# Kernel optimization log

Measured on AMD Instinct MI355X. Metric: run time of the kernel, lower is better.

The kernel has to match this reference:

```python
import jax, jax.numpy as jnp
import numpy as np
import math

# --- config (OctoConfig defaults) ---
OBS_H = 2
STATE_DIM = 2
N_LAYER = 12
N_HEAD = 6
N_EMBD = 384
IMG = 96
PATCH = 8
N_IMG_TOK = (IMG // PATCH) ** 2          # 144
TOT_TOK = OBS_H * (N_IMG_TOK + 1) + 1    # 291
HEAD_DIM = N_EMBD // N_HEAD
LN_EPS = 1e-5
B = 128


def _sinusoidal_pos_embed(n_position, d_hid):
    position = np.arange(n_position)[:, None].astype(np.float32)
    div_term = np.exp(np.arange(0, d_hid, 2).astype(np.float32) * -(math.log(10000.0) / d_hid))
    pe = np.zeros((1, n_position, d_hid), dtype=np.float32)
    pe[0, :, 0::2] = np.sin(position * div_term)
    pe[0, :, 1::2] = np.cos(position * div_term)
    return jnp.asarray(pe)


def setup_inputs() -> dict:
    key = jax.random.key(0)
    ks = jax.random.split(key, 16)
    std = 0.02
    inp = {}
    inp['images'] = jax.random.normal(ks[0], (B, OBS_H, 3, IMG, IMG), jnp.float32)
    inp['agent_state'] = jax.random.normal(ks[1], (B, OBS_H, STATE_DIM), jnp.float32)
    # image tokenizer
    inp['img_proj_w'] = jax.random.normal(ks[2], (PATCH * PATCH * 3, N_EMBD), jnp.float32) * std
    inp['img_proj_b'] = jnp.zeros((N_EMBD,), jnp.float32)
    inp['img_temb'] = jax.random.normal(ks[3], (1, OBS_H, 1, N_EMBD), jnp.float32)
    # agent-state tokenizer MLP: state_dim -> 32 -> n_embd
    inp['st_w1'] = jax.random.normal(ks[4], (STATE_DIM, 32), jnp.float32) * std
    inp['st_b1'] = jnp.zeros((32,), jnp.float32)
    inp['st_w2'] = jax.random.normal(ks[5], (32, N_EMBD), jnp.float32) * std
    inp['st_b2'] = jnp.zeros((N_EMBD,), jnp.float32)
    inp['st_temb'] = jax.random.normal(ks[6], (1, OBS_H, 1, N_EMBD), jnp.float32)
    inp['readout'] = jax.random.normal(ks[7], (1, 1, N_EMBD), jnp.float32)
    inp['pos_embed'] = _sinusoidal_pos_embed(TOT_TOK, N_EMBD)
    # stacked per-layer transformer params (leading dim = N_LAYER), scanned
    L = N_LAYER
    inp['ln1_w'] = jnp.ones((L, N_EMBD), jnp.float32)
    inp['ln1_b'] = jnp.zeros((L, N_EMBD), jnp.float32)
    inp['attn_w'] = jax.random.normal(ks[8], (L, N_EMBD, 3 * N_EMBD), jnp.float32) * std
    inp['attn_b'] = jnp.zeros((L, 3 * N_EMBD), jnp.float32)
    inp['attn_proj_w'] = jax.random.normal(ks[9], (L, N_EMBD, N_EMBD), jnp.float32) * std
    inp['attn_proj_b'] = jnp.zeros((L, N_EMBD), jnp.float32)
    inp['ln2_w'] = jnp.ones((L, N_EMBD), jnp.float32)
    inp['ln2_b'] = jnp.zeros((L, N_EMBD), jnp.float32)
    inp['fc_w'] = jax.random.normal(ks[10], (L, N_EMBD, 4 * N_EMBD), jnp.float32) * std
    inp['fc_b'] = jnp.zeros((L, 4 * N_EMBD), jnp.float32)
    inp['fc2_w'] = jax.random.normal(ks[11], (L, 4 * N_EMBD, N_EMBD), jnp.float32) * std
    inp['fc2_b'] = jnp.zeros((L, N_EMBD), jnp.float32)
    inp['lnf_w'] = jnp.ones((N_EMBD,), jnp.float32)
    inp['lnf_b'] = jnp.zeros((N_EMBD,), jnp.float32)
    return inp


def _layernorm(x, w, b):
    m = jnp.mean(x, axis=-1, keepdims=True)
    v = jnp.mean((x - m) ** 2, axis=-1, keepdims=True)
    return (x - m) * jax.lax.rsqrt(v + LN_EPS) * w + b


def _forward(images, agent_state, img_proj_w, img_proj_b, img_temb,
             st_w1, st_b1, st_w2, st_b2, st_temb, readout, pos_embed,
             ln1_w, ln1_b, attn_w, attn_b, attn_proj_w, attn_proj_b,
             ln2_w, ln2_b, fc_w, fc_b, fc2_w, fc2_b, lnf_w, lnf_b):
    Bn, T, C, H, W = images.shape
    p = PATCH
    # --- ImageTokenizer: patchify (B*T, n_patches, p*p*C) then project ---
    x = images.reshape(Bn * T, C, H // p, p, W // p, p)
    x = x.transpose(0, 2, 4, 3, 5, 1).reshape(Bn * T, -1, p * p * C)
    img_tok = x @ img_proj_w + img_proj_b
    img_tok = img_tok.reshape(Bn, T, -1, N_EMBD) + img_temb  # [B,T,144,D]
    # --- AgentStateTokenizer ---
    st = jax.nn.relu(agent_state @ st_w1 + st_b1) @ st_w2 + st_b2
    st_tok = st.reshape(Bn, T, 1, N_EMBD) + st_temb          # [B,T,1,D]
    # --- combine + readout + positional ---
    combined = jnp.concatenate([st_tok, img_tok], axis=2).reshape(Bn, -1, N_EMBD)
    ro = jnp.broadcast_to(readout, (Bn, 1, N_EMBD))
    x = jnp.concatenate([combined, ro], axis=1) + pos_embed  # [B,291,D]
    Ttot = x.shape[1]
    # custom mask: all-visible except last (readout) row attends only to itself
    neg = jnp.float32(-jnp.inf)
    bias = jnp.zeros((Ttot, Ttot), jnp.float32).at[-1, :-1].set(neg)
    scale = 1.0 / math.sqrt(HEAD_DIM + 1e-8)

    def block(h, params):
        (l1w, l1b, aw, ab, pw, pb, l2w, l2b, fw, fb, f2w, f2b) = params
        y = _layernorm(h, l1w, l1b)
        qkv = y @ aw + ab
        q, k, v = jnp.split(qkv, 3, axis=-1)
        q = q.reshape(Bn, Ttot, N_HEAD, HEAD_DIM)
        k = k.reshape(Bn, Ttot, N_HEAD, HEAD_DIM)
        v = v.reshape(Bn, Ttot, N_HEAD, HEAD_DIM)
        scores = jnp.einsum('bqhd,bkhd->bhqk', q, k) * scale + bias
        attn = jax.nn.softmax(scores, axis=-1)
        o = jnp.einsum('bhqk,bkhd->bqhd', attn, v).reshape(Bn, Ttot, N_EMBD)
        h = h + o @ pw + pb
        y2 = _layernorm(h, l2w, l2b)
        h = h + jax.nn.gelu(y2 @ fw + fb, approximate=True) @ f2w + f2b
        return h, None

    layer_params = (ln1_w, ln1_b, attn_w, attn_b, attn_proj_w, attn_proj_b,
                    ln2_w, ln2_b, fc_w, fc_b, fc2_w, fc2_b)
    x, _ = jax.lax.scan(block, x, layer_params)
    x = _layernorm(x, lnf_w, lnf_b)
    return x[:, -1]  # readout token embedding [B, D]


def reference(images, agent_state, img_proj_w, img_proj_b, img_temb,
              st_w1, st_b1, st_w2, st_b2, st_temb, readout, pos_embed,
              ln1_w, ln1_b, attn_w, attn_b, attn_proj_w, attn_proj_b,
              ln2_w, ln2_b, fc_w, fc_b, fc2_w, fc2_b, lnf_w, lnf_b):
    return _forward(images, agent_state, img_proj_w, img_proj_b, img_temb,
                    st_w1, st_b1, st_w2, st_b2, st_temb, readout, pos_embed,
                    ln1_w, ln1_b, attn_w, attn_b, attn_proj_w, attn_proj_b,
                    ln2_w, ln2_b, fc_w, fc_b, fc2_w, fc2_b, lnf_w, lnf_b)
```

## Files before the change

kernel.cpp:

```cpp
#include <hip/hip_runtime.h>

typedef unsigned short u16;
typedef unsigned int u32;

typedef __bf16 bf16x8 __attribute__((ext_vector_type(8)));
typedef float  f32x4  __attribute__((ext_vector_type(4)));

#define N_EMBD 384
#define TT     291
#define NB     128

__device__ __forceinline__ u16 f2bf(float x) {
    union { float f; u32 u; } v; v.f = x;
    u32 r = v.u + 0x7FFFu + ((v.u >> 16) & 1u);
    return (u16)(r >> 16);
}
__device__ __forceinline__ float bfl(u32 u) { return __uint_as_float(u << 16); }
__device__ __forceinline__ float bfh(u32 u) { return __uint_as_float(u & 0xFFFF0000u); }

__device__ __forceinline__ float gelu_f(float x) {
    float u = 0.7978845608028654f * x * (1.f + 0.044715f * x * x);
    float e = __expf(2.f * u);
    float t = 1.f - 2.f / (e + 1.f);
    return 0.5f * x * (1.f + t);
}

__device__ __forceinline__ void load16_lds(const u16* g, u16* l) {
    __builtin_amdgcn_global_load_lds(
        (const __attribute__((address_space(1))) u32*)g,
        (__attribute__((address_space(3))) u32*)l, 16, 0, 0);
}

__device__ __forceinline__ void tr_tile(const float* __restrict__ src,
                                        u16* __restrict__ dst,
                                        int R, int C, int r0, int c0, int tid) {
    __shared__ float tile[32][33];
    int cc = tid & 31, rr0 = tid >> 5;
#pragma unroll
    for (int s = 0; s < 4; ++s) {
        int rr = rr0 + s * 8;
        tile[rr][cc] = src[(size_t)(r0 + rr) * C + c0 + cc];
    }
    __syncthreads();
#pragma unroll
    for (int s = 0; s < 4; ++s) {
        int rr = rr0 + s * 8;
        dst[(size_t)(c0 + rr) * R + (r0 + cc)] = f2bf(tile[cc][rr]);
    }
}

__global__ __launch_bounds__(256) void transpose_cvt(const float* __restrict__ in,
                                                     u16* __restrict__ out, int R, int C) {
    tr_tile(in, out, R, C, blockIdx.y * 32, blockIdx.x * 32, threadIdx.x);
}

__global__ __launch_bounds__(256) void transpose_layer(const float* __restrict__ attn_w,
                                                       const float* __restrict__ proj_w,
                                                       const float* __restrict__ fc_w,
                                                       const float* __restrict__ fc2_w,
                                                       u16* __restrict__ wqkv,
                                                       u16* __restrict__ wproj,
                                                       u16* __restrict__ wfc,
                                                       u16* __restrict__ wfc2t,
                                                       int l) {
    int t = blockIdx.x;
    const float* src; u16* dst; int R, C, tx, ty;
    if (t < 432)       { int i = t;        src = attn_w + (size_t)l * 384 * 1152; dst = wqkv;  R = 384;  C = 1152; tx = i % 36; ty = i / 36; }
    else if (t < 576)  { int i = t - 432;  src = proj_w + (size_t)l * 384 * 384;  dst = wproj; R = 384;  C = 384;  tx = i % 12; ty = i / 12; }
    else if (t < 1152) { int i = t - 576;  src = fc_w   + (size_t)l * 384 * 1536; dst = wfc;   R = 384;  C = 1536; tx = i % 48; ty = i / 48; }
    else               { int i = t - 1152; src = fc2_w  + (size_t)l * 1536 * 384; dst = wfc2t; R = 1536; C = 384;  tx = i % 12; ty = i / 12; }
    tr_tile(src, dst, R, C, ty * 32, tx * 32, threadIdx.x);
}

template<int MODE>
__global__ __launch_bounds__(256) void gemm_bt(const u16* __restrict__ A,
                                               const u16* __restrict__ BT, int ldb,
                                               const float* __restrict__ bias,
                                               void* __restrict__ out,
                                               const float* __restrict__ resid,
                                               int N, int K) {
    __shared__ u16 As[128 * 64];
    __shared__ u16 Bs[128 * 64];
    int tid = threadIdx.x;
    int lane = tid & 63, wave = tid >> 6;
    int wr = wave >> 1, wc = wave & 1;

    int nwg  = gridDim.x * gridDim.y;
    int orig = blockIdx.y * gridDim.x + blockIdx.x;
    int qq = nwg >> 3, rr = nwg & 7;
    int xcd = orig & 7, idx0 = orig >> 3;
    int wg = (xcd < rr ? xcd * (qq + 1) : rr * (qq + 1) + (xcd - rr) * qq) + idx0;
    int bx = wg % gridDim.x, by = wg / gridDim.x;

    const u16* Ab = A  + (size_t)by * 128 * K;
    const u16* Bb = BT + (size_t)bx * 128 * ldb;

    f32x4 acc[4][4];
#pragma unroll
    for (int i = 0; i < 4; ++i)
#pragma unroll
        for (int j = 0; j < 4; ++j)
#pragma unroll
            for (int r = 0; r < 4; ++r) acc[i][j][r] = 0.f;

    int r16  = lane & 15;
    int quad = lane >> 4;
    int sw   = r16 & 7;

    int srow[4], scol[4];
#pragma unroll
    for (int s = 0; s < 4; ++s) {
        int seg = s * 256 + tid;
        srow[s] = seg >> 3;
        scol[s] = (((seg & 7) ^ (srow[s] & 7)) << 3);
    }

    for (int kt = 0; kt < K; kt += 64) {
#pragma unroll
        for (int s = 0; s < 4; ++s) {
            int seg = s * 256 + tid;
            load16_lds(Ab + (size_t)srow[s] * K   + kt + scol[s], &As[seg * 8]);
            load16_lds(Bb + (size_t)srow[s] * ldb + kt + scol[s], &Bs[seg * 8]);
        }
        __syncthreads();
#pragma unroll
        for (int kk = 0; kk < 2; ++kk) {
            bf16x8 af[4], bff[4];
#pragma unroll
            for (int i = 0; i < 4; ++i) {
                int cg = ((kk * 4 + quad) ^ sw) << 3;
                af[i]  = *(const bf16x8*)&As[(wr * 64 + i * 16 + r16) * 64 + cg];
                bff[i] = *(const bf16x8*)&Bs[(wc * 64 + i * 16 + r16) * 64 + cg];
            }
#pragma unroll
            for (int i = 0; i < 4; ++i)
#pragma unroll
                for (int j = 0; j < 4; ++j)
                    acc[i][j] = __builtin_amdgcn_mfma_f32_16x16x32_bf16(af[i], bff[j], acc[i][j], 0, 0, 0);
        }
        __syncthreads();
    }

    int rbase = (lane >> 4) * 4;
#pragma unroll
    for (int i = 0; i < 4; ++i) {
#pragma unroll
        for (int j = 0; j < 4; ++j) {
            int gr0 = by * 128 + wr * 64 + i * 16 + rbase;
            int gc  = bx * 128 + wc * 64 + j * 16 + (lane & 15);
            float bj = bias ? bias[gc] : 0.f;
#pragma unroll
            for (int r = 0; r < 4; ++r) {
                size_t idx = (size_t)(gr0 + r) * N + gc;
                float v = acc[i][j][r] + bj;
                if (MODE == 0)      ((u16*)out)[idx] = f2bf(v);
                else if (MODE == 1) ((u16*)out)[idx] = f2bf(gelu_f(v));
                else if (MODE == 2) ((float*)out)[idx] = resid[idx] + v;
                else                ((float*)out)[idx] = v;
            }
        }
    }
}

template<bool BF16OUT>
__global__ __launch_bounds__(256) void ln_kernel(const float* __restrict__ x,
                                                 const float* __restrict__ w,
                                                 const float* __restrict__ b,
                                                 void* __restrict__ yout,
                                                 int inRowMul, int inRowAdd, int nRows) {
    int row = blockIdx.x * 4 + (threadIdx.x >> 6);
    if (row >= nRows) return;
    const float* xr = x + ((size_t)row * inRowMul + inRowAdd) * N_EMBD;
    int lane = threadIdx.x & 63;
    float v[6], s = 0.f, s2 = 0.f;
#pragma unroll
    for (int i = 0; i < 6; ++i) {
        v[i] = xr[lane + 64 * i];
        s += v[i]; s2 += v[i] * v[i];
    }
#pragma unroll
    for (int off = 32; off > 0; off >>= 1) {
        s  += __shfl_down(s, off);
        s2 += __shfl_down(s2, off);
    }
    float mean = __shfl(s, 0) * (1.f / 384.f);
    float var  = __shfl(s2, 0) * (1.f / 384.f) - mean * mean;
    float rs = rsqrtf(var + 1e-5f);
#pragma unroll
    for (int i = 0; i < 6; ++i) {
        int c = lane + 64 * i;
        float o = (v[i] - mean) * rs * w[c] + b[c];
        if (BF16OUT) ((u16*)yout)[(size_t)row * N_EMBD + c] = f2bf(o);
        else         ((float*)yout)[(size_t)row * N_EMBD + c] = o;
    }
}

__global__ __launch_bounds__(512) void attn_mfma(const u16* __restrict__ qkv,
                                                 u16* __restrict__ o) {
    __shared__ __align__(16) u16 Ks[304 * 64];
    __shared__ __align__(16) u16 Vt[64 * 328];
    __shared__ __align__(16) u16 Ps[8 * 16 * 40];
    int h = blockIdx.x, b = blockIdx.y;
    int tid = threadIdx.x;
    int lane = tid & 63, wave = tid >> 6;
    int ln = lane & 15, quad = lane >> 4;
    int sw = ln & 7;
    const u16* base = qkv + (size_t)b * TT * 1152;

    for (int c = tid; c < 304 * 8; c += 512) {
        int row = c >> 3;
        int g   = (c & 7) ^ (row & 7);
        int srow = row < TT ? row : TT - 1;
        load16_lds(base + (size_t)srow * 1152 + 384 + h * 64 + g * 8, &Ks[c * 8]);
    }
    for (int s = tid; s < TT * 8; s += 512) {
        int dg = s / TT, k = s - dg * TT;
        uint4 v = *(const uint4*)(base + (size_t)k * 1152 + 768 + h * 64 + dg * 8);
        const u16* pv = (const u16*)&v;
#pragma unroll
        for (int j = 0; j < 8; ++j) Vt[(dg * 8 + j) * 328 + k] = pv[j];
    }
    for (int s = tid; s < 64 * 37; s += 512) {
        int d = s / 37, c2 = s - d * 37;
        Vt[d * 328 + TT + c2] = 0;
    }
    __syncthreads();

    for (int qt = wave; qt < 19; qt += 8) {
        int q0 = qt * 16;
        int qrow = q0 + ln; if (qrow > TT - 1) qrow = TT - 1;
        const u16* qp = base + (size_t)qrow * 1152 + h * 64;
        bf16x8 qf0 = *(const bf16x8*)(qp + quad * 8);
        bf16x8 qf1 = *(const bf16x8*)(qp + 32 + quad * 8);

        f32x4 sc[19];
#pragma unroll
        for (int kt = 0; kt < 19; ++kt) {
            const u16* kr = &Ks[(kt * 16 + ln) * 64];
            bf16x8 kb0 = *(const bf16x8*)&kr[(quad ^ sw) << 3];
            bf16x8 kb1 = *(const bf16x8*)&kr[((4 | quad) ^ sw) << 3];
            f32x4 z = {0.f, 0.f, 0.f, 0.f};
            z = __builtin_amdgcn_mfma_f32_16x16x32_bf16(qf0, kb0, z, 0, 0, 0);
            sc[kt] = __builtin_amdgcn_mfma_f32_16x16x32_bf16(qf1, kb1, z, 0, 0, 0);
        }

        const float C = 0.18033688011112042f;
        float linv[4];
#pragma unroll
        for (int r = 0; r < 4; ++r) {
            float m = -1e30f;
            if (qt == 18) {
                int q = q0 + quad * 4 + r;
#pragma unroll
                for (int kt = 0; kt < 19; ++kt) {
                    int key = kt * 16 + ln;
                    bool ok = (key < TT) && (q != TT - 1 || key == TT - 1);
                    float s = ok ? sc[kt][r] : -1e30f;
                    sc[kt][r] = s;
                    m = fmaxf(m, s);
                }
            } else {
#pragma unroll
                for (int kt = 0; kt < 18; ++kt) m = fmaxf(m, sc[kt][r]);
                float s = (288 + ln < TT) ? sc[18][r] : -1e30f;
                sc[18][r] = s;
                m = fmaxf(m, s);
            }
            m = fmaxf(m, __shfl_xor(m, 1));
            m = fmaxf(m, __shfl_xor(m, 2));
            m = fmaxf(m, __shfl_xor(m, 4));
            m = fmaxf(m, __shfl_xor(m, 8));
            float mc = m * C;
            float l = 0.f;
#pragma unroll
            for (int kt = 0; kt < 19; ++kt) {
                float p = __builtin_amdgcn_exp2f(fmaf(sc[kt][r], C, -mc));
                sc[kt][r] = p;
                l += p;
            }
            l += __shfl_xor(l, 1);
            l += __shfl_xor(l, 2);
            l += __shfl_xor(l, 4);
            l += __shfl_xor(l, 8);
            linv[r] = 1.f / l;
        }

        u16* Pw = &Ps[wave * 16 * 40];
        f32x4 of[4];
#pragma unroll
        for (int nt = 0; nt < 4; ++nt)
#pragma unroll
            for (int r = 0; r < 4; ++r) of[nt][r] = 0.f;
#pragma unroll
        for (int kt2 = 0; kt2 < 10; ++kt2) {
#pragma unroll
            for (int half = 0; half < 2; ++half) {
                int kt = kt2 * 2 + half;
#pragma unroll
                for (int r = 0; r < 4; ++r) {
                    float v = (kt < 19) ? sc[kt][r] : 0.f;
                    Pw[(quad * 4 + r) * 40 + half * 16 + ln] = f2bf(v);
                }
            }
            bf16x8 pa = *(const bf16x8*)&Pw[ln * 40 + quad * 8];
#pragma unroll
            for (int nt = 0; nt < 4; ++nt) {
                bf16x8 vb = *(const bf16x8*)&Vt[(nt * 16 + ln) * 328 + kt2 * 32 + quad * 8];
                of[nt] = __builtin_amdgcn_mfma_f32_16x16x32_bf16(pa, vb, of[nt], 0, 0, 0);
            }
        }

#pragma unroll
        for (int nt = 0; nt < 4; ++nt) {
#pragma unroll
            for (int r = 0; r < 4; ++r) {
                int q = q0 + quad * 4 + r;
                if (q < TT)
                    o[((size_t)(b * TT + q)) * N_EMBD + h * 64 + nt * 16 + ln] =
                        f2bf(of[nt][r] * linv[r]);
            }
        }
    }
}

__global__ __launch_bounds__(256) void patchify_kernel(const float* __restrict__ images,
                                                       u16* __restrict__ P) {
    int idx = blockIdx.x * 256 + threadIdx.x;
    int col = idx % 192, row = idx / 192;
    int p = row % 144, bt = row / 144;
    int c = col % 3, pp = col / 3;
    int pw = pp & 7, ph = pp >> 3;
    int hp = p / 12, wp = p % 12;
    float v = images[(((size_t)bt * 3 + c) * 96 + hp * 8 + ph) * 96 + wp * 8 + pw];
    P[idx] = f2bf(v);
}

__global__ __launch_bounds__(256) void img_scatter_kernel(const float* __restrict__ imgtok,
                                                          const float* __restrict__ temb,
                                                          const float* __restrict__ pos,
                                                          float* __restrict__ xw) {
    int idx = blockIdx.x * 256 + threadIdx.x;
    int n = idx % 384, row = idx / 384;
    int p = row % 144, bt = row / 144;
    int t = bt & 1, b = bt >> 1;
    int tok = t * 145 + 1 + p;
    xw[((size_t)b * TT + tok) * N_EMBD + n] =
        imgtok[idx] + temb[t * N_EMBD + n] + pos[(size_t)tok * N_EMBD + n];
}

__global__ __launch_bounds__(384) void st_kernel(const float* __restrict__ state,
                                                 const float* __restrict__ w1,
                                                 const float* __restrict__ b1,
                                                 const float* __restrict__ w2,
                                                 const float* __restrict__ b2,
                                                 const float* __restrict__ temb,
                                                 const float* __restrict__ pos,
                                                 float* __restrict__ xw) {
    int bt = blockIdx.x;
    int t = bt & 1, b = bt >> 1;
    int n = threadIdx.x;
    float s0 = state[bt * 2], s1 = state[bt * 2 + 1];
    float acc = b2[n];
#pragma unroll
    for (int j = 0; j < 32; ++j) {
        float hh = fmaxf(s0 * w1[j] + s1 * w1[32 + j] + b1[j], 0.f);
        acc += hh * w2[j * N_EMBD + n];
    }
    int tok = t * 145;
    xw[((size_t)b * TT + tok) * N_EMBD + n] =
        acc + temb[t * N_EMBD + n] + pos[(size_t)tok * N_EMBD + n];
}

__global__ __launch_bounds__(256) void ro_kernel(const float* __restrict__ readout,
                                                 const float* __restrict__ pos,
                                                 float* __restrict__ xw) {
    int idx = blockIdx.x * 256 + threadIdx.x;
    int n = idx % 384, b = idx / 384;
    xw[((size_t)b * TT + 290) * N_EMBD + n] = readout[n] + pos[(size_t)290 * N_EMBD + n];
}

extern "C" void kernel_launch(void* const* d_in, const int* in_sizes, int n_in,
                              void* d_out, int out_size, void* d_ws, size_t ws_size,
                              hipStream_t stream) {
    const float* images   = (const float*)d_in[0];
    const float* state    = (const float*)d_in[1];
    const float* img_w    = (const float*)d_in[2];
    const float* img_b    = (const float*)d_in[3];
    const float* img_temb = (const float*)d_in[4];
    const float* st_w1    = (const float*)d_in[5];
    const float* st_b1    = (const float*)d_in[6];
    const float* st_w2    = (const float*)d_in[7];
    const float* st_b2    = (const float*)d_in[8];
    const float* st_temb  = (const float*)d_in[9];
    const float* readout  = (const float*)d_in[10];
    const float* pos      = (const float*)d_in[11];
    const float* ln1_w    = (const float*)d_in[12];
    const float* ln1_b    = (const float*)d_in[13];
    const float* attn_w   = (const float*)d_in[14];
    const float* attn_b   = (const float*)d_in[15];
    const float* proj_w   = (const float*)d_in[16];
    const float* proj_b   = (const float*)d_in[17];
    const float* ln2_w    = (const float*)d_in[18];
    const float* ln2_b    = (const float*)d_in[19];
    const float* fc_w     = (const float*)d_in[20];
    const float* fc_b     = (const float*)d_in[21];
    const float* fc2_w    = (const float*)d_in[22];
    const float* fc2_b    = (const float*)d_in[23];
    const float* lnf_w    = (const float*)d_in[24];
    const float* lnf_b    = (const float*)d_in[25];

    char* ws = (char*)d_ws;
    float* XW   = (float*)(ws);
    u16*   Y    = (u16*)(ws + 57212928ull);
    u16*   SH   = (u16*)(ws + 85819392ull);
    u16*   QKV  = SH;
    u16*   G    = SH;
    u16*   P    = SH;
    float* IMGT = (float*)(ws + 85819392ull + 14155776ull);
    u16*   WQKVl  = (u16*)(ws + 171638784ull);
    u16*   WPROJl = (u16*)(ws + 172523520ull);
    u16*   WFCl   = (u16*)(ws + 172818432ull);
    u16*   WFC2Tl = (u16*)(ws + 173998080ull);
    u16*   WIMG   = (u16*)(ws + 175177728ull);

    transpose_cvt<<<dim3(12, 6), 256, 0, stream>>>(img_w, WIMG, 192, 384);
    patchify_kernel<<<27648, 256, 0, stream>>>(images, P);
    gemm_bt<3><<<dim3(3, 288), 256, 0, stream>>>(P, WIMG, 192, img_b, IMGT, nullptr, 384, 192);
    img_scatter_kernel<<<55296, 256, 0, stream>>>(IMGT, img_temb, pos, XW);
    st_kernel<<<256, 384, 0, stream>>>(state, st_w1, st_b1, st_w2, st_b2, st_temb, pos, XW);
    ro_kernel<<<192, 256, 0, stream>>>(readout, pos, XW);

    const size_t M0 = 18688;
    for (int l = 0; l < 12; ++l) {
        transpose_layer<<<1728, 256, 0, stream>>>(attn_w, proj_w, fc_w, fc2_w,
                                                  WQKVl, WPROJl, WFCl, WFC2Tl, l);
        ln_kernel<true><<<9312, 256, 0, stream>>>(XW, ln1_w + l * 384, ln1_b + l * 384, Y, 1, 0, 37248);
        gemm_bt<0><<<dim3(9, 291), 256, 0, stream>>>(Y, WQKVl, 384, attn_b + l * 1152,
                                                     QKV, nullptr, 1152, 384);
        attn_mfma<<<dim3(6, 128), 512, 0, stream>>>(QKV, Y);
        gemm_bt<2><<<dim3(3, 291), 256, 0, stream>>>(Y, WPROJl, 384, proj_b + l * 384,
                                                     XW, XW, 384, 384);
        ln_kernel<true><<<9312, 256, 0, stream>>>(XW, ln2_w + l * 384, ln2_b + l * 384, Y, 1, 0, 37248);
        gemm_bt<1><<<dim3(12, 146), 256, 0, stream>>>(Y, WFCl, 384, fc_b + l * 1536,
                                                      G, nullptr, 1536, 384);
        gemm_bt<2><<<dim3(3, 146), 256, 0, stream>>>(G, WFC2Tl, 1536, fc2_b + l * 384,
                                                     XW, XW, 384, 1536);
        gemm_bt<1><<<dim3(12, 145), 256, 0, stream>>>(Y + M0 * 384, WFCl, 384, fc_b + l * 1536,
                                                      G, nullptr, 1536, 384);
        gemm_bt<2><<<dim3(3, 145), 256, 0, stream>>>(G, WFC2Tl, 1536, fc2_b + l * 384,
                                                     XW + M0 * 384, XW + M0 * 384, 384, 1536);
    }
    ln_kernel<false><<<32, 256, 0, stream>>>(XW, lnf_w, lnf_b, d_out, TT, 290, 128);
}
```

Baseline: 4.385 ms.

## Compute transposed attention scores to feed P directly from registers

The QK^T MFMA now swaps operands so each lane holds scores for one query across 4 consecutive keys. The probabilities can then be converted to bf16 in registers and used directly as the A operand of 16x16x16 MFMAs for PV, removing the per-wave LDS staging buffer for P. Row max and sum reductions drop from 4 rows × 4 shuffles to 2 shuffles per lane, and the 1/l factor is redistributed with shuffles. It also sets a min-blocks launch bound, and it uses twice as many narrower MFMAs for PV and keeps 19 packed P vectors in registers, which adds register pressure.

```diff
diff --git a/kernel.cpp b/kernel.cpp
--- a/kernel.cpp
+++ b/kernel.cpp
@@ -5,6 +5,7 @@
 
 typedef __bf16 bf16x8 __attribute__((ext_vector_type(8)));
 typedef float  f32x4  __attribute__((ext_vector_type(4)));
+typedef short  s16x4  __attribute__((ext_vector_type(4)));
 
 #define N_EMBD 384
 #define TT     291
@@ -23,6 +24,20 @@
     float e = __expf(2.f * u);
     float t = 1.f - 2.f / (e + 1.f);
     return 0.5f * x * (1.f + t);
+}
+
+__device__ __forceinline__ f32x4 mfma16(s16x4 a, s16x4 b, f32x4 c) {
+#if __has_builtin(__builtin_amdgcn_mfma_f32_16x16x16bf16_1k)
+    return __builtin_amdgcn_mfma_f32_16x16x16bf16_1k(a, b, c, 0, 0, 0);
+#elif __has_builtin(__builtin_amdgcn_mfma_f32_16x16x16_bf16)
+    typedef __bf16 bf16x4v __attribute__((ext_vector_type(4)));
+    return __builtin_amdgcn_mfma_f32_16x16x16_bf16(__builtin_bit_cast(bf16x4v, a),
+                                                   __builtin_bit_cast(bf16x4v, b), c, 0, 0, 0);
+#else
+    f32x4 d = c;
+    asm("v_mfma_f32_16x16x16_bf16 %0, %1, %2, %0" : "+v"(d) : "v"(a), "v"(b));
+    return d;
+#endif
 }
 
 __device__ __forceinline__ void load16_lds(const u16* g, u16* l) {
@@ -195,11 +210,10 @@
     }
 }
 
-__global__ __launch_bounds__(512) void attn_mfma(const u16* __restrict__ qkv,
-                                                 u16* __restrict__ o) {
+__global__ __launch_bounds__(512, 4) void attn_mfma(const u16* __restrict__ qkv,
+                                                    u16* __restrict__ o) {
     __shared__ __align__(16) u16 Ks[304 * 64];
     __shared__ __align__(16) u16 Vt[64 * 328];
-    __shared__ __align__(16) u16 Ps[8 * 16 * 40];
     int h = blockIdx.x, b = blockIdx.y;
     int tid = threadIdx.x;
     int lane = tid & 63, wave = tid >> 6;
@@ -240,86 +254,81 @@
             bf16x8 kb0 = *(const bf16x8*)&kr[(quad ^ sw) << 3];
             bf16x8 kb1 = *(const bf16x8*)&kr[((4 | quad) ^ sw) << 3];
             f32x4 z = {0.f, 0.f, 0.f, 0.f};
-            z = __builtin_amdgcn_mfma_f32_16x16x32_bf16(qf0, kb0, z, 0, 0, 0);
-            sc[kt] = __builtin_amdgcn_mfma_f32_16x16x32_bf16(qf1, kb1, z, 0, 0, 0);
+            z = __builtin_amdgcn_mfma_f32_16x16x32_bf16(kb0, qf0, z, 0, 0, 0);
+            sc[kt] = __builtin_amdgcn_mfma_f32_16x16x32_bf16(kb1, qf1, z, 0, 0, 0);
         }
 
         const float C = 0.18033688011112042f;
-        float linv[4];
-#pragma unroll
-        for (int r = 0; r < 4; ++r) {
-            float m = -1e30f;
-            if (qt == 18) {
-                int q = q0 + quad * 4 + r;
-#pragma unroll
-                for (int kt = 0; kt < 19; ++kt) {
-                    int key = kt * 16 + ln;
+        int q = q0 + ln;
+        float m = -1e30f;
+        if (qt == 18) {
+#pragma unroll
+            for (int kt = 0; kt < 19; ++kt)
+#pragma unroll
+                for (int r = 0; r < 4; ++r) {
+                    int key = kt * 16 + quad * 4 + r;
                     bool ok = (key < TT) && (q != TT - 1 || key == TT - 1);
                     float s = ok ? sc[kt][r] : -1e30f;
                     sc[kt][r] = s;
                     m = fmaxf(m, s);
                 }
-            } else {
-#pragma unroll
-                for (int kt = 0; kt < 18; ++kt) m = fmaxf(m, sc[kt][r]);
-                float s = (288 + ln < TT) ? sc[18][r] : -1e30f;
+        } else {
+#pragma unroll
+            for (int kt = 0; kt < 18; ++kt)
+#pragma unroll
+                for (int r = 0; r < 4; ++r) m = fmaxf(m, sc[kt][r]);
+#pragma unroll
+            for (int r = 0; r < 4; ++r) {
+                int key = 288 + quad * 4 + r;
+                float s = (key < TT) ? sc[18][r] : -1e30f;
                 sc[18][r] = s;
                 m = fmaxf(m, s);
             }
-            m = fmaxf(m, __shfl_xor(m, 1));
-            m = fmaxf(m, __shfl_xor(m, 2));
-            m = fmaxf(m, __shfl_xor(m, 4));
-            m = fmaxf(m, __shfl_xor(m, 8));
-            float mc = m * C;
-            float l = 0.f;
-#pragma unroll
-            for (int kt = 0; kt < 19; ++kt) {
+        }
+        m = fmaxf(m, __shfl_xor(m, 16));
+        m = fmaxf(m, __shfl_xor(m, 32));
+
+        float mc = m * C;
+        float l = 0.f;
+        s16x4 pa[19];
+#pragma unroll
+        for (int kt = 0; kt < 19; ++kt)
+#pragma unroll
+            for (int r = 0; r < 4; ++r) {
                 float p = __builtin_amdgcn_exp2f(fmaf(sc[kt][r], C, -mc));
-                sc[kt][r] = p;
                 l += p;
-            }
-            l += __shfl_xor(l, 1);
-            l += __shfl_xor(l, 2);
-            l += __shfl_xor(l, 4);
-            l += __shfl_xor(l, 8);
-            linv[r] = 1.f / l;
-        }
-
-        u16* Pw = &Ps[wave * 16 * 40];
+                pa[kt][r] = (short)f2bf(p);
+            }
+        l += __shfl_xor(l, 16);
+        l += __shfl_xor(l, 32);
+        float linv = 1.f / l;
+        float linvq[4];
+#pragma unroll
+        for (int r = 0; r < 4; ++r) linvq[r] = __shfl(linv, quad * 4 + r);
+
         f32x4 of[4];
 #pragma unroll
         for (int nt = 0; nt < 4; ++nt)
 #pragma unroll
             for (int r = 0; r < 4; ++r) of[nt][r] = 0.f;
 #pragma unroll
-        for (int kt2 = 0; kt2 < 10; ++kt2) {
-#pragma unroll
-            for (int half = 0; half < 2; ++half) {
-                int kt = kt2 * 2 + half;
-#pragma unroll
-                for (int r = 0; r < 4; ++r) {
-                    float v = (kt < 19) ? sc[kt][r] : 0.f;
-                    Pw[(quad * 4 + r) * 40 + half * 16 + ln] = f2bf(v);
-                }
-            }
-            bf16x8 pa = *(const bf16x8*)&Pw[ln * 40 + quad * 8];
+        for (int kt = 0; kt < 19; ++kt) {
 #pragma unroll
             for (int nt = 0; nt < 4; ++nt) {
-                bf16x8 vb = *(const bf16x8*)&Vt[(nt * 16 + ln) * 328 + kt2 * 32 + quad * 8];
-                of[nt] = __builtin_amdgcn_mfma_f32_16x16x32_bf16(pa, vb, of[nt], 0, 0, 0);
-            }
-        }
-
-#pragma unroll
-        for (int nt = 0; nt < 4; ++nt) {
+                s16x4 vb = *(const s16x4*)&Vt[(nt * 16 + ln) * 328 + kt * 16 + quad * 4];
+                of[nt] = mfma16(pa[kt], vb, of[nt]);
+            }
+        }
+
+#pragma unroll
+        for (int nt = 0; nt < 4; ++nt)
 #pragma unroll
             for (int r = 0; r < 4; ++r) {
-                int q = q0 + quad * 4 + r;
-                if (q < TT)
-                    o[((size_t)(b * TT + q)) * N_EMBD + h * 64 + nt * 16 + ln] =
-                        f2bf(of[nt][r] * linv[r]);
-            }
-        }
+                int qo = q0 + quad * 4 + r;
+                if (qo < TT)
+                    o[((size_t)(b * TT + qo)) * N_EMBD + h * 64 + nt * 16 + ln] =
+                        f2bf(of[nt][r] * linvq[r]);
+            }
     }
 }
 
```

New measurement: 8.125 ms. 1.85x slower.
